# Performance work log

Hardware: AMD Instinct MI355X
Metric: run time of the kernel (lower is better)

The kernel has to match this reference:

```python
import jax, jax.numpy as jnp
import numpy as np

N, E, F_IN, F_E = 50000, 800000, 128, 16
R, H, C = 4, 4, 32            # num_relations, heads, out_channels
HC = H * C                     # 128
NEG_SLOPE = 0.2                # PyG RGATConv default negative_slope
EPS = 1e-16                    # PyG softmax epsilon


def rgat_conv(x, src, dst, edge_type, edge_attr, w, q, k, e, le, b, concat):
    """Faithful PyG RGATConv (additive-self-attention, across-relation, dim=1, aggr=add).
    x: [N,F]; w: [R,F,H*C]; q,k,e: [H*C,H]; le: [F_e,H*C]; b: bias."""
    n = x.shape[0]
    xw = jnp.einsum('nf,rfo->rno', x, w)              # [R,N,H*C] per-relation projections
    x_i = xw[edge_type, dst]                          # [E,H*C] target-node proj per edge
    x_j = xw[edge_type, src]                          # [E,H*C] source-node proj per edge
    qi = x_i @ q                                      # [E,H]
    kj = x_j @ k + (edge_attr @ le) @ e               # [E,H] (edge features folded into keys)
    alpha = jax.nn.leaky_relu(qi + kj, NEG_SLOPE)     # [E,H]
    # softmax over incoming edges of each destination node (across relations)
    amax = jax.ops.segment_max(alpha, dst, num_segments=n)
    ex = jnp.exp(alpha - amax[dst])
    denom = jax.ops.segment_sum(ex, dst, num_segments=n)
    alpha = ex / (denom[dst] + EPS)
    msg = alpha[:, :, None] * x_j.reshape(-1, H, C)   # [E,H,C]
    out = jax.ops.segment_sum(msg, dst, num_segments=n)  # [N,H,C] sum aggregation
    out = out.reshape(n, H * C) if concat else out.mean(axis=1)
    return out + b


def setup_inputs() -> dict:
    key = jax.random.key(0)
    ks = jax.random.split(key, 18)
    p = 0.05
    inp = {
        'x': jax.random.normal(ks[0], (N, F_IN), dtype=jnp.float32),
        'edge_index': jax.random.randint(ks[1], (2, E), 0, N, dtype=jnp.int64)
            if jax.config.jax_enable_x64 else jax.random.randint(ks[1], (2, E), 0, N).astype(jnp.int32),
        'edge_attr': jax.random.normal(ks[2], (E, F_E), dtype=jnp.float32),
        'edge_type': jax.random.randint(ks[3], (E,), 0, R).astype(jnp.int32),
        # conv1 params (in=F_IN, concat=True -> bias of size H*C)
        'w1': jax.random.normal(ks[4], (R, F_IN, HC), dtype=jnp.float32) * p,
        'q1': jax.random.normal(ks[5], (HC, H), dtype=jnp.float32) * p,
        'k1': jax.random.normal(ks[6], (HC, H), dtype=jnp.float32) * p,
        'e1': jax.random.normal(ks[7], (HC, H), dtype=jnp.float32) * p,
        'le1': jax.random.normal(ks[8], (F_E, HC), dtype=jnp.float32) * p,
        'b1': jnp.zeros((HC,), dtype=jnp.float32),
        # conv3 params (in=H*C=128, concat=False -> bias of size C)
        'w3': jax.random.normal(ks[9], (R, HC, HC), dtype=jnp.float32) * p,
        'q3': jax.random.normal(ks[10], (HC, H), dtype=jnp.float32) * p,
        'k3': jax.random.normal(ks[11], (HC, H), dtype=jnp.float32) * p,
        'e3': jax.random.normal(ks[12], (HC, H), dtype=jnp.float32) * p,
        'le3': jax.random.normal(ks[13], (F_E, HC), dtype=jnp.float32) * p,
        'b3': jnp.zeros((C,), dtype=jnp.float32),
    }
    return inp


def reference(x, edge_index, edge_attr, edge_type,
              w1, q1, k1, e1, le1, b1,
              w3, q3, k3, e3, le3, b3):
    src, dst = edge_index[0], edge_index[1]
    h = jax.nn.relu(rgat_conv(x, src, dst, edge_type, edge_attr,
                              w1, q1, k1, e1, le1, b1, concat=True))
    out = rgat_conv(h, src, dst, edge_type, edge_attr,
                    w3, q3, k3, e3, le3, b3, concat=False)
    return out
```

## Files before the change

kernel.cpp:

```cpp
#include <hip/hip_runtime.h>


#define NEG_SLOPE 0.2f
#define SOFT_EPS 1e-16f

typedef __attribute__((ext_vector_type(8))) short bf16x8;
typedef __attribute__((ext_vector_type(4))) float f32x4;
typedef __attribute__((ext_vector_type(4))) unsigned short u16x4;
typedef __attribute__((ext_vector_type(4))) _Float16 half4;
typedef __attribute__((ext_vector_type(8))) _Float16 half8;

__device__ __forceinline__ void bf16split(float f, unsigned short& h, unsigned short& l) {
  unsigned u = __float_as_uint(f);
  unsigned r = u + 0x7FFFu + ((u >> 16) & 1u);
  h = (unsigned short)(r >> 16);
  float fh = __uint_as_float(((unsigned)h) << 16);
  float d = f - fh;
  unsigned u2 = __float_as_uint(d);
  unsigned r2 = u2 + 0x7FFFu + ((u2 >> 16) & 1u);
  l = (unsigned short)(r2 >> 16);
}


__device__ __forceinline__ void hist_body(int id, const int* __restrict__ dst,
                                          int* __restrict__ deg, int E) {
  int e = id * 256 + (int)threadIdx.x;
  if (e < E) atomicAdd(&deg[dst[e]], 1);
}

__device__ __forceinline__ void convx_body(int id, const float* __restrict__ in,
                                           unsigned short* __restrict__ hi,
                                           unsigned short* __restrict__ lo, int total8) {
  int i = id * 256 + (int)threadIdx.x;
  if (i >= total8) return;
  const float4* p = (const float4*)in + (size_t)i * 2;
  float4 a = p[0], b = p[1];
  float v[8] = {a.x, a.y, a.z, a.w, b.x, b.y, b.z, b.w};
  bf16x8 hv, lv;
#pragma unroll
  for (int j = 0; j < 8; ++j) {
    unsigned short h, l;
    bf16split(v[j], h, l);
    hv[j] = (short)h; lv[j] = (short)l;
  }
  *(bf16x8*)(hi + (size_t)i * 8) = hv;
  *(bf16x8*)(lo + (size_t)i * 8) = lv;
}

__device__ __forceinline__ void convw_body(int idx, const float* __restrict__ w1,
                                           const float* __restrict__ w3,
                                           unsigned short* __restrict__ whiT1,
                                           unsigned short* __restrict__ wloT1,
                                           unsigned short* __restrict__ whiT3,
                                           unsigned short* __restrict__ wloT3) {
  if (idx >= 131072) return;
  int L = idx >> 16;
  int rem = idx & 65535;
  int r = rem >> 14, rem2 = rem & 16383, f = rem2 >> 7, o = rem2 & 127;
  const float* w = L ? w3 : w1;
  unsigned short* hiT = L ? whiT3 : whiT1;
  unsigned short* loT = L ? wloT3 : wloT1;
  float v = w[(r * 128 + f) * 128 + o];
  unsigned short h, l;
  bf16split(v, h, l);
  hiT[(r * 128 + o) * 128 + f] = h;
  loT[(r * 128 + o) * 128 + f] = l;
}

__device__ __forceinline__ void wqk_body(int idx, const float* __restrict__ w1,
                                         const float* __restrict__ q1, const float* __restrict__ k1,
                                         const float* __restrict__ w3, const float* __restrict__ q3,
                                         const float* __restrict__ k3, float* __restrict__ wqk) {
  if (idx >= 8192) return;
  int L = idx >> 12, rem = idx & 4095;
  int r = rem >> 10, rem2 = rem & 1023, f = rem2 >> 3, j = rem2 & 7;
  const float* w = L ? w3 : w1;
  const float* qk = (j < 4) ? (L ? q3 : q1) : (L ? k3 : k1);
  int h = j & 3;
  const float* wrow = w + (r * 128 + f) * 128;
  float acc = 0.f;
  for (int o = 0; o < 128; ++o) acc += wrow[o] * qk[o * 4 + h];
  wqk[idx] = acc;
}

__device__ __forceinline__ void lee_body(const float* __restrict__ le1, const float* __restrict__ e1,
                                         const float* __restrict__ le3, const float* __restrict__ e3,
                                         float* __restrict__ lee) {
  int t = threadIdx.x;
  if (t >= 128) return;
  const float* le = (t < 64) ? le1 : le3;
  const float* ee = (t < 64) ? e1 : e3;
  int u = t & 63, f = u >> 2, h = u & 3;
  float acc = 0.f;
  for (int o = 0; o < 128; ++o) acc += le[f * 128 + o] * ee[o * 4 + h];
  lee[t] = acc;
}

__global__ __launch_bounds__(256) void pre_kernel(
    const int* __restrict__ dst, int* __restrict__ deg, int E,
    const float* __restrict__ x, unsigned short* __restrict__ xhi,
    unsigned short* __restrict__ xlo, int total8,
    const float* __restrict__ w1, const float* __restrict__ q1, const float* __restrict__ k1,
    const float* __restrict__ w3, const float* __restrict__ q3, const float* __restrict__ k3,
    float* __restrict__ wqk,
    const float* __restrict__ le1, const float* __restrict__ e1,
    const float* __restrict__ le3, const float* __restrict__ e3, float* __restrict__ lee,
    unsigned short* __restrict__ whiT1, unsigned short* __restrict__ wloT1,
    unsigned short* __restrict__ whiT3, unsigned short* __restrict__ wloT3,
    int nAB, int eb, int cxb) {
  int bid = blockIdx.x;
  if (bid < nAB) {
    int id = bid >> 1;
    if (bid & 1) {
      if (id < eb) hist_body(id, dst, deg, E);
    } else {
      if (id < cxb) convx_body(id, x, xhi, xlo, total8);
    }
  } else {
    int b2 = bid - nAB;
    if (b2 < 512) {
      convw_body(b2 * 256 + (int)threadIdx.x, w1, w3, whiT1, wloT1, whiT3, wloT3);
    } else if (b2 < 544) {
      wqk_body((b2 - 512) * 256 + (int)threadIdx.x, w1, q1, k1, w3, q3, k3, wqk);
    } else {
      lee_body(le1, e1, le3, e3, lee);
    }
  }
}


__global__ __launch_bounds__(256) void scanA_kernel(const int* __restrict__ deg,
                                                    int* __restrict__ bsum, int N) {
  int b = blockIdx.x, t = threadIdx.x;
  int base = b * 1024 + t * 4;
  int s = 0;
#pragma unroll
  for (int j = 0; j < 4; ++j) {
    int i = base + j;
    if (i < N) s += deg[i];
  }
#pragma unroll
  for (int o = 1; o < 64; o <<= 1) s += __shfl_xor(s, o);
  __shared__ int wsum[4];
  if ((t & 63) == 0) wsum[t >> 6] = s;
  __syncthreads();
  if (t == 0) bsum[b] = wsum[0] + wsum[1] + wsum[2] + wsum[3];
}

__global__ __launch_bounds__(256) void scanB_kernel(const int* __restrict__ bsum,
                                                    int* __restrict__ boff,
                                                    int* __restrict__ row_start,
                                                    int nb, int N) {
  int t = threadIdx.x;
  int v = (t < nb) ? bsum[t] : 0;
  int inc = v;
#pragma unroll
  for (int o = 1; o < 64; o <<= 1) {
    int u = __shfl_up(inc, o);
    if ((t & 63) >= o) inc += u;
  }
  __shared__ int wt[4];
  if ((t & 63) == 63) wt[t >> 6] = inc;
  __syncthreads();
  int add = 0;
  for (int wv = 0; wv < (t >> 6); ++wv) add += wt[wv];
  inc += add;
  if (t < nb) boff[t] = inc - v;
  if (t == 255) row_start[N] = inc;
}

__global__ __launch_bounds__(256) void scanC_kernel(const int* __restrict__ deg,
                                                    const int* __restrict__ boff,
                                                    int* __restrict__ row_start,
                                                    int* __restrict__ cursor, int N) {
  int b = blockIdx.x, t = threadIdx.x;
  int base = b * 1024 + t * 4;
  int d[4];
  int s = 0;
#pragma unroll
  for (int j = 0; j < 4; ++j) {
    int i = base + j;
    d[j] = (i < N) ? deg[i] : 0;
    s += d[j];
  }
  int inc = s;
#pragma unroll
  for (int o = 1; o < 64; o <<= 1) {
    int u = __shfl_up(inc, o);
    if ((t & 63) >= o) inc += u;
  }
  __shared__ int wt[4];
  if ((t & 63) == 63) wt[t >> 6] = inc;
  __syncthreads();
  int add = boff[b];
  for (int wv = 0; wv < (t >> 6); ++wv) add += wt[wv];
  int off = add + inc - s;
#pragma unroll
  for (int j = 0; j < 4; ++j) {
    int i = base + j;
    if (i < N) {
      row_start[i] = off;
      cursor[i] = off;
      off += d[j];
    }
  }
}


__device__ __forceinline__ void scatter_body(int id, const int* __restrict__ src,
                                             const int* __restrict__ dst,
                                             const int* __restrict__ et,
                                             int* __restrict__ cursor,
                                             int4* __restrict__ es, int E) {
  int e = id * 256 + (int)threadIdx.x;
  if (e >= E) return;
  int d = dst[e];
  int pos = atomicAdd(&cursor[d], 1);
  es[pos] = make_int4(src[e], d, et[e], e);
}

__device__ __forceinline__ void qkx_body(int nbid, char* smem, const float* __restrict__ xin,
                                         const float* __restrict__ wqk, float* __restrict__ qn,
                                         float* __restrict__ kn, int N) {
  float* sx = (float*)smem;
  float* swqk = sx + 64 * 132;
  int nb = nbid * 64;
  int t = threadIdx.x;
#pragma unroll
  for (int j = 0; j < 16; ++j) {
    int i = j * 256 + t;
    swqk[(i >> 10) * 1032 + (i & 1023)] = wqk[i];
  }
#pragma unroll
  for (int j = 0; j < 8; ++j) {
    int i = j * 256 + t;
    int n = nb + (i >> 5); if (n >= N) n = N - 1;
    ((float4*)sx)[(i >> 5) * 33 + (i & 31)] =
        ((const float4*)(xin + (size_t)n * 128))[i & 31];
  }
  __syncthreads();
  int rl = t >> 2, r = t & 3;
  float aq0 = 0, aq1 = 0, aq2 = 0, aq3 = 0;
  float ak0 = 0, ak1 = 0, ak2 = 0, ak3 = 0;
  const float* xr = sx + rl * 132;
  const float* wb = swqk + r * 1032;
  for (int f = 0; f < 128; ++f) {
    float xv = xr[f];
    float4 qw = *(const float4*)(wb + f * 8);
    float4 kw = *(const float4*)(wb + f * 8 + 4);
    aq0 += xv * qw.x; aq1 += xv * qw.y; aq2 += xv * qw.z; aq3 += xv * qw.w;
    ak0 += xv * kw.x; ak1 += xv * kw.y; ak2 += xv * kw.z; ak3 += xv * kw.w;
  }
  int n = nb + rl;
  if (n < N) {
    *(float4*)(qn + ((size_t)r * N + n) * 4) = make_float4(aq0, aq1, aq2, aq3);
    *(float4*)(kn + ((size_t)r * N + n) * 4) = make_float4(ak0, ak1, ak2, ak3);
  }
}

__global__ __launch_bounds__(256) void sc_kernel(
    const int* __restrict__ src, const int* __restrict__ dst, const int* __restrict__ et,
    int* __restrict__ cursor, int4* __restrict__ es, int E,
    const float* __restrict__ xin, const float* __restrict__ wqk,
    float* __restrict__ qn, float* __restrict__ kn, int N, int qxb) {
  extern __shared__ char smem[];
  int bid = blockIdx.x;
  int g = bid / 5, r5 = bid - g * 5;
  if (r5 == 4) {
    if (g < qxb) qkx_body(g, smem, xin, wqk, qn, kn, N);
  } else {
    scatter_body(g * 4 + r5, src, dst, et, cursor, es, E);
  }
}


__device__ __forceinline__ void ek2_body(int id, char* smem, const int4* __restrict__ es,
                                         const float* __restrict__ ea,
                                         const float* __restrict__ lee,
                                         float* __restrict__ eks1, float* __restrict__ eks3,
                                         int E) {
  float* sl = (float*)smem;
  if (threadIdx.x < 128) sl[threadIdx.x] = lee[threadIdx.x];
  __syncthreads();
  int i = id * 256 + (int)threadIdx.x;
  if (i >= E) return;
  int eid = es[i].w;
  const float4* a4 = (const float4*)(ea + (size_t)eid * 16);
  float a1[4] = {0, 0, 0, 0}, a3[4] = {0, 0, 0, 0};
#pragma unroll
  for (int ii = 0; ii < 4; ++ii) {
    float4 v = a4[ii];
    int f = ii * 4;
#pragma unroll
    for (int h = 0; h < 4; ++h) {
      a1[h] += v.x * sl[f * 4 + h] + v.y * sl[(f + 1) * 4 + h] +
               v.z * sl[(f + 2) * 4 + h] + v.w * sl[(f + 3) * 4 + h];
      a3[h] += v.x * sl[64 + f * 4 + h] + v.y * sl[64 + (f + 1) * 4 + h] +
               v.z * sl[64 + (f + 2) * 4 + h] + v.w * sl[64 + (f + 3) * 4 + h];
    }
  }
  *(float4*)(eks1 + (size_t)i * 4) = make_float4(a1[0], a1[1], a1[2], a1[3]);
  *(float4*)(eks3 + (size_t)i * 4) = make_float4(a3[0], a3[1], a3[2], a3[3]);
}

__device__ __forceinline__ void proj_body(int pid, char* smem,
                                          const unsigned short* __restrict__ xhi,
                                          const unsigned short* __restrict__ xlo,
                                          const unsigned short* __restrict__ whiT,
                                          const unsigned short* __restrict__ wloT,
                                          _Float16* __restrict__ xwh, int N) {
  bf16x8* wl_h = (bf16x8*)smem;
  bf16x8* wl_l = wl_h + 2048;
  int r = pid & 3;
  int nb = (pid >> 2) * 128;
  int t = threadIdx.x;
  const unsigned short* wh = whiT + r * (128 * 128);
  const unsigned short* wl = wloT + r * (128 * 128);

#pragma unroll
  for (int j = 0; j < 8; ++j) {
    int i = j * 256 + t;
    int c = i & 15, q = (i >> 4) & 3, kc = (i >> 6) & 3, ot = i >> 8;
    int srco = (ot * 16 + c) * 128 + kc * 32 + q * 8;
    wl_h[i] = *(const bf16x8*)(wh + srco);
    wl_l[i] = *(const bf16x8*)(wl + srco);
  }
  __syncthreads();

  int wv = t >> 6;
  int lane = t & 63;
  int c = lane & 15, q = lane >> 4;
  int nodebase = nb + wv * 32;
  int n0 = nodebase + c;
  int n1 = nodebase + 16 + c;
  int n0c = n0 < N ? n0 : N - 1;
  int n1c = n1 < N ? n1 : N - 1;

  f32x4 acc[8][2];
#pragma unroll
  for (int ot = 0; ot < 8; ++ot)
#pragma unroll
    for (int nt = 0; nt < 2; ++nt) acc[ot][nt] = (f32x4){0.f, 0.f, 0.f, 0.f};

  bf16x8 xb[2][4];
  {
    int k0 = q * 8;
    xb[0][0] = *(const bf16x8*)(xhi + (size_t)n0c * 128 + k0);
    xb[0][1] = *(const bf16x8*)(xlo + (size_t)n0c * 128 + k0);
    xb[0][2] = *(const bf16x8*)(xhi + (size_t)n1c * 128 + k0);
    xb[0][3] = *(const bf16x8*)(xlo + (size_t)n1c * 128 + k0);
  }
#pragma unroll
  for (int kc = 0; kc < 4; ++kc) {
    if (kc < 3) {
      int k0 = (kc + 1) * 32 + q * 8;
      xb[(kc + 1) & 1][0] = *(const bf16x8*)(xhi + (size_t)n0c * 128 + k0);
      xb[(kc + 1) & 1][1] = *(const bf16x8*)(xlo + (size_t)n0c * 128 + k0);
      xb[(kc + 1) & 1][2] = *(const bf16x8*)(xhi + (size_t)n1c * 128 + k0);
      xb[(kc + 1) & 1][3] = *(const bf16x8*)(xlo + (size_t)n1c * 128 + k0);
    }
    bf16x8 b0h = xb[kc & 1][0], b0l = xb[kc & 1][1];
    bf16x8 b1h = xb[kc & 1][2], b1l = xb[kc & 1][3];
#pragma unroll
    for (int ot = 0; ot < 8; ++ot) {
      int fi = ((ot * 4 + kc) * 4 + q) * 16 + c;
      bf16x8 ah = wl_h[fi];
      bf16x8 al = wl_l[fi];
      acc[ot][0] = __builtin_amdgcn_mfma_f32_16x16x32_bf16(ah, b0h, acc[ot][0], 0, 0, 0);
      acc[ot][0] = __builtin_amdgcn_mfma_f32_16x16x32_bf16(ah, b0l, acc[ot][0], 0, 0, 0);
      acc[ot][0] = __builtin_amdgcn_mfma_f32_16x16x32_bf16(al, b0h, acc[ot][0], 0, 0, 0);
      acc[ot][1] = __builtin_amdgcn_mfma_f32_16x16x32_bf16(ah, b1h, acc[ot][1], 0, 0, 0);
      acc[ot][1] = __builtin_amdgcn_mfma_f32_16x16x32_bf16(ah, b1l, acc[ot][1], 0, 0, 0);
      acc[ot][1] = __builtin_amdgcn_mfma_f32_16x16x32_bf16(al, b1h, acc[ot][1], 0, 0, 0);
    }
  }

#pragma unroll
  for (int nt = 0; nt < 2; ++nt) {
    int n = nodebase + nt * 16 + c;
    if (n < N) {
      _Float16* basep = xwh + ((size_t)r * N + n) * 128 + q * 4;
#pragma unroll
      for (int ot = 0; ot < 8; ++ot) {
        f32x4 a = acc[ot][nt];
        half4 hv;
        hv[0] = (_Float16)a.x; hv[1] = (_Float16)a.y;
        hv[2] = (_Float16)a.z; hv[3] = (_Float16)a.w;
        *(half4*)(basep + ot * 16) = hv;
      }
    }
  }
}

__global__ __launch_bounds__(256) void ep1_kernel(
    const int4* __restrict__ es, const float* __restrict__ ea, const float* __restrict__ lee,
    float* __restrict__ eks1, float* __restrict__ eks3, int E,
    const unsigned short* __restrict__ xhi, const unsigned short* __restrict__ xlo,
    const unsigned short* __restrict__ whiT, const unsigned short* __restrict__ wloT,
    _Float16* __restrict__ xwh, int N, int pjb) {
  extern __shared__ char smem[];
  int bid = blockIdx.x;
  int g = bid / 3, r3 = bid - g * 3;
  if (r3 == 2) {
    if (g < pjb) proj_body(g, smem, xhi, xlo, whiT, wloT, xwh, N);
  } else {
    ek2_body(g * 2 + r3, smem, es, ea, lee, eks1, eks3, E);
  }
}

__global__ __launch_bounds__(256) void p2_kernel(
    const unsigned short* __restrict__ xhi, const unsigned short* __restrict__ xlo,
    const unsigned short* __restrict__ whiT, const unsigned short* __restrict__ wloT,
    _Float16* __restrict__ xwh, int N,
    const float* __restrict__ xin, const float* __restrict__ wqk,
    float* __restrict__ qn, float* __restrict__ kn, int pjb, int qxb) {
  extern __shared__ char smem[];
  int bid = blockIdx.x;
  int g = bid / 3, r3 = bid - g * 3;
  if (r3 == 2) {
    if (g < qxb) qkx_body(g, smem, xin, wqk, qn, kn, N);
  } else {
    int id = g * 2 + r3;
    if (id < pjb) proj_body(id, smem, xhi, xlo, whiT, wloT, xwh, N);
  }
}


__device__ __forceinline__ float4 edge_alpha(const int4* __restrict__ es,
                                             const float* __restrict__ qn,
                                             const float* __restrict__ kn,
                                             const float* __restrict__ eks,
                                             int i, int d, int N) {
  int4 v = es[i];
  float4 kv = *(const float4*)(kn + (v.z * N + v.x) * 4);
  float4 ev = ((const float4*)eks)[i];
  float4 q4 = *(const float4*)(qn + (v.z * N + d) * 4);
  float4 a = make_float4(q4.x + kv.x + ev.x, q4.y + kv.y + ev.y,
                         q4.z + kv.z + ev.z, q4.w + kv.w + ev.w);
  a.x = a.x > 0.f ? a.x : NEG_SLOPE * a.x;
  a.y = a.y > 0.f ? a.y : NEG_SLOPE * a.y;
  a.z = a.z > 0.f ? a.z : NEG_SLOPE * a.z;
  a.w = a.w > 0.f ? a.w : NEG_SLOPE * a.w;
  return a;
}

__device__ __forceinline__ float4 max4(float4 a, float4 b) {
  return make_float4(fmaxf(a.x, b.x), fmaxf(a.y, b.y), fmaxf(a.z, b.z), fmaxf(a.w, b.w));
}

__global__ __launch_bounds__(256) void agg_kernel(
    const int4* __restrict__ es, const int* __restrict__ row_start,
    const float* __restrict__ qn, const float* __restrict__ kn,
    const float* __restrict__ eks, float* __restrict__ alpha_s,
    const _Float16* __restrict__ xwh, const float* __restrict__ bias,
    float* __restrict__ out, unsigned short* __restrict__ xhi,
    unsigned short* __restrict__ xlo, int N, int concat) {
  int d = blockIdx.x * 16 + (threadIdx.x >> 4);
  if (d >= N) return;
  int ql = threadIdx.x & 15;
  int rs = row_start[d], re = row_start[d + 1];
  int deg = re - rs;
  int h = ql >> 2;

  float acc[8];
#pragma unroll
  for (int j = 0; j < 8; ++j) acc[j] = 0.f;
  float rden = 0.f;

  if (deg > 0) {
    float4 m = make_float4(-1e30f, -1e30f, -1e30f, -1e30f);
    float4 ar0 = m, ar1 = m, ar2 = m, ar3 = m;
    bool fast = (deg <= 64);
    bool v0 = ql < deg, v1 = 16 + ql < deg, v2 = 32 + ql < deg, v3 = 48 + ql < deg;
    if (fast) {
      int dm1 = deg - 1;
      int o0 = v0 ? ql : dm1;
      int o1 = v1 ? 16 + ql : dm1;
      int o2 = v2 ? 32 + ql : dm1;
      int o3 = v3 ? 48 + ql : dm1;
      float4 a0 = edge_alpha(es, qn, kn, eks, rs + o0, d, N);
      float4 a1 = edge_alpha(es, qn, kn, eks, rs + o1, d, N);
      float4 a2 = edge_alpha(es, qn, kn, eks, rs + o2, d, N);
      float4 a3 = edge_alpha(es, qn, kn, eks, rs + o3, d, N);
      if (v0) { ar0 = a0; m = max4(m, a0); }
      if (v1) { ar1 = a1; m = max4(m, a1); }
      if (v2) { ar2 = a2; m = max4(m, a2); }
      if (v3) { ar3 = a3; m = max4(m, a3); }
    } else {
      for (int i = rs + ql; i < re; i += 16) {
        float4 a = edge_alpha(es, qn, kn, eks, i, d, N);
        ((float4*)alpha_s)[i] = a;
        m = max4(m, a);
      }
    }
#pragma unroll
    for (int o = 1; o < 16; o <<= 1) {
      m.x = fmaxf(m.x, __shfl_xor(m.x, o));
      m.y = fmaxf(m.y, __shfl_xor(m.y, o));
      m.z = fmaxf(m.z, __shfl_xor(m.z, o));
      m.w = fmaxf(m.w, __shfl_xor(m.w, o));
    }

    float4 s = make_float4(0.f, 0.f, 0.f, 0.f);
    if (fast) {
#define SWEEPB(V, AR, OFF)                                                   \
      if (V) {                                                               \
        float4 e4 = make_float4(__expf(AR.x - m.x), __expf(AR.y - m.y),      \
                                __expf(AR.z - m.z), __expf(AR.w - m.w));     \
        ((float4*)alpha_s)[rs + OFF + ql] = e4;                              \
        s.x += e4.x; s.y += e4.y; s.z += e4.z; s.w += e4.w;                  \
      }
      SWEEPB(v0, ar0, 0)
      SWEEPB(v1, ar1, 16)
      SWEEPB(v2, ar2, 32)
      SWEEPB(v3, ar3, 48)
#undef SWEEPB
    } else {
      for (int i = rs + ql; i < re; i += 16) {
        float4 a = ((const float4*)alpha_s)[i];
        float4 e4 = make_float4(__expf(a.x - m.x), __expf(a.y - m.y),
                                __expf(a.z - m.z), __expf(a.w - m.w));
        ((float4*)alpha_s)[i] = e4;
        s.x += e4.x; s.y += e4.y; s.z += e4.z; s.w += e4.w;
      }
    }
#pragma unroll
    for (int o = 1; o < 16; o <<= 1) {
      s.x += __shfl_xor(s.x, o); s.y += __shfl_xor(s.y, o);
      s.z += __shfl_xor(s.z, o); s.w += __shfl_xor(s.w, o);
    }
    float smh = (h == 0) ? s.x : (h == 1) ? s.y : (h == 2) ? s.z : s.w;
    rden = 1.f / (smh + SOFT_EPS);

    int e = rs;
    for (; e + 4 <= re; e += 4) {
      int4 a0 = es[e];
      int4 a1 = es[e + 1];
      int4 a2 = es[e + 2];
      int4 a3 = es[e + 3];
      float w0 = alpha_s[e * 4 + h];
      float w1 = alpha_s[(e + 1) * 4 + h];
      float w2 = alpha_s[(e + 2) * 4 + h];
      float w3 = alpha_s[(e + 3) * 4 + h];
      half8 x0 = *(const half8*)(xwh + (a0.z * N + a0.x) * 128 + ql * 8);
      half8 x1 = *(const half8*)(xwh + (a1.z * N + a1.x) * 128 + ql * 8);
      half8 x2 = *(const half8*)(xwh + (a2.z * N + a2.x) * 128 + ql * 8);
      half8 x3 = *(const half8*)(xwh + (a3.z * N + a3.x) * 128 + ql * 8);
#pragma unroll
      for (int j = 0; j < 8; ++j) {
        acc[j] = fmaf((float)x0[j], w0, acc[j]);
        acc[j] = fmaf((float)x1[j], w1, acc[j]);
        acc[j] = fmaf((float)x2[j], w2, acc[j]);
        acc[j] = fmaf((float)x3[j], w3, acc[j]);
      }
    }
    for (; e < re; ++e) {
      int4 a0 = es[e];
      float w0 = alpha_s[e * 4 + h];
      half8 x0 = *(const half8*)(xwh + (a0.z * N + a0.x) * 128 + ql * 8);
#pragma unroll
      for (int j = 0; j < 8; ++j) acc[j] = fmaf((float)x0[j], w0, acc[j]);
    }
  }
#pragma unroll
  for (int j = 0; j < 8; ++j) acc[j] *= rden;

  if (concat) {
    float4 b0 = ((const float4*)bias)[ql * 2];
    float4 b1 = ((const float4*)bias)[ql * 2 + 1];
    float v[8] = {acc[0] + b0.x, acc[1] + b0.y, acc[2] + b0.z, acc[3] + b0.w,
                  acc[4] + b1.x, acc[5] + b1.y, acc[6] + b1.z, acc[7] + b1.w};
    u16x4 hv0, lv0, hv1, lv1;
#pragma unroll
    for (int j = 0; j < 8; ++j) {
      v[j] = v[j] > 0.f ? v[j] : 0.f;
      unsigned short hh, ll;
      bf16split(v[j], hh, ll);
      if (j < 4) { hv0[j] = hh; lv0[j] = ll; }
      else { hv1[j - 4] = hh; lv1[j - 4] = ll; }
    }
    float* orow = out + (size_t)d * 128 + ql * 8;
    *(float4*)orow = make_float4(v[0], v[1], v[2], v[3]);
    *(float4*)(orow + 4) = make_float4(v[4], v[5], v[6], v[7]);
    *(u16x4*)(xhi + (size_t)d * 128 + ql * 8) = hv0;
    *(u16x4*)(xhi + (size_t)d * 128 + ql * 8 + 4) = hv1;
    *(u16x4*)(xlo + (size_t)d * 128 + ql * 8) = lv0;
    *(u16x4*)(xlo + (size_t)d * 128 + ql * 8 + 4) = lv1;
  } else {
#pragma unroll
    for (int j = 0; j < 8; ++j) {
      acc[j] += __shfl_xor(acc[j], 4);
      acc[j] += __shfl_xor(acc[j], 8);
    }
    if (ql < 4) {
      float4 b0 = ((const float4*)bias)[ql * 2];
      float4 b1 = ((const float4*)bias)[ql * 2 + 1];
      float* orow = out + (size_t)d * 32 + ql * 8;
      *(float4*)orow = make_float4(0.25f * acc[0] + b0.x, 0.25f * acc[1] + b0.y,
                                   0.25f * acc[2] + b0.z, 0.25f * acc[3] + b0.w);
      *(float4*)(orow + 4) = make_float4(0.25f * acc[4] + b1.x, 0.25f * acc[5] + b1.y,
                                         0.25f * acc[6] + b1.z, 0.25f * acc[7] + b1.w);
    }
  }
}

extern "C" void kernel_launch(void* const* d_in, const int* in_sizes, int n_in,
                              void* d_out, int out_size, void* d_ws, size_t ws_size,
                              hipStream_t stream) {
  const float* x   = (const float*)d_in[0];
  const int*   ei  = (const int*)d_in[1];
  const float* ea  = (const float*)d_in[2];
  const int*   etp = (const int*)d_in[3];
  const float* w1  = (const float*)d_in[4];
  const float* q1  = (const float*)d_in[5];
  const float* k1  = (const float*)d_in[6];
  const float* e1  = (const float*)d_in[7];
  const float* le1 = (const float*)d_in[8];
  const float* b1  = (const float*)d_in[9];
  const float* w3  = (const float*)d_in[10];
  const float* q3  = (const float*)d_in[11];
  const float* k3  = (const float*)d_in[12];
  const float* e3  = (const float*)d_in[13];
  const float* le3 = (const float*)d_in[14];
  const float* b3  = (const float*)d_in[15];
  const int N = in_sizes[0] / 128;
  const int E = in_sizes[3];
  const int* srcp = ei;
  const int* dstp = ei + E;

  float* ws   = (float*)d_ws;
  _Float16* xwh = (_Float16*)ws;
  float* qn   = ws + (size_t)2 * N * 128;
  float* kn   = qn + (size_t)4 * N * 4;
  float* eks1 = kn + (size_t)4 * N * 4;
  float* eks3 = eks1 + (size_t)E * 4;
  float* alph = eks3 + (size_t)E * 4;
  float* hbuf = alph + (size_t)E * 4;
  float* leeb = hbuf + (size_t)N * 128;
  float* wqkb = leeb + 128;
  int* deg      = (int*)(wqkb + 8192);
  int* rowst    = deg + N;
  int* cursor   = rowst + N + 1;
  int* bsum     = cursor + N;
  int* boff     = bsum + 256;
  uintptr_t pe = (uintptr_t)(boff + 256);
  pe = (pe + 15) & ~(uintptr_t)15;
  int4* es      = (int4*)pe;
  uintptr_t pa = (uintptr_t)(es + E);
  pa = (pa + 255) & ~(uintptr_t)255;
  unsigned short* xhi   = (unsigned short*)pa;
  unsigned short* xlo   = xhi + (size_t)N * 128;
  unsigned short* whiT1 = xlo + (size_t)N * 128;
  unsigned short* wloT1 = whiT1 + 4 * 128 * 128;
  unsigned short* whiT3 = wloT1 + 4 * 128 * 128;
  unsigned short* wloT3 = whiT3 + 4 * 128 * 128;
  (void)ws_size; (void)n_in; (void)out_size;

  int eb   = (E + 255) / 256;
  int nb16 = (N + 15) / 16;
  int nbs  = (N + 1023) / 1024;
  int pgy  = (N + 127) / 128;
  int pjb  = 4 * pgy;
  int qxb  = (N + 63) / 64;
  int cxb  = (N * 128 / 8 + 255) / 256;

  hipMemsetAsync(deg, 0, (size_t)N * sizeof(int), stream);

  int M = eb > cxb ? eb : cxb;
  int nAB = 2 * M;
  int preg = nAB + 512 + 32 + 1;
  pre_kernel<<<preg, 256, 0, stream>>>(dstp, deg, E, x, xhi, xlo, N * 128 / 8,
                                       w1, q1, k1, w3, q3, k3, wqkb,
                                       le1, e1, le3, e3, leeb,
                                       whiT1, wloT1, whiT3, wloT3, nAB, eb, cxb);
  scanA_kernel<<<nbs, 256, 0, stream>>>(deg, bsum, N);
  scanB_kernel<<<1, 256, 0, stream>>>(bsum, boff, rowst, nbs, N);
  scanC_kernel<<<nbs, 256, 0, stream>>>(deg, boff, rowst, cursor, N);

  int scq = (eb + 3) / 4;
  int scg = 5 * (scq > qxb ? scq : qxb);
  sc_kernel<<<scg, 256, 50304, stream>>>(srcp, dstp, etp, cursor, es, E,
                                         x, wqkb, qn, kn, N, qxb);

  int ekh = (eb + 1) / 2;
  int e1g = 3 * (ekh > pjb ? ekh : pjb);
  ep1_kernel<<<e1g, 256, 65536, stream>>>(es, ea, leeb, eks1, eks3, E,
                                          xhi, xlo, whiT1, wloT1, xwh, N, pjb);

  agg_kernel<<<nb16, 256, 0, stream>>>(es, rowst, qn, kn, eks1, alph, xwh,
                                       b1, hbuf, xhi, xlo, N, 1);

  int pjh = (pjb + 1) / 2;
  int p2g = 3 * (pjh > qxb ? pjh : qxb);
  p2_kernel<<<p2g, 256, 65536, stream>>>(xhi, xlo, whiT3, wloT3, xwh, N,
                                         hbuf, wqkb + 4096, qn, kn, pjb, qxb);

  agg_kernel<<<nb16, 256, 0, stream>>>(es, rowst, qn, kn, eks3, alph, xwh,
                                       b3, (float*)d_out, xhi, xlo, N, 0);
}
```

Before: 441.0 us.

## Pre-swizzle weights to MFMA fragment order and drop LDS staging to cut shared memory

The bf16 hi/lo weight split is now written directly in the per-lane MFMA fragment layout, so the projection reads A-fragments straight from global/L2 instead of staging 64KB into LDS and syncing. The q/k node projection also reads x rows directly from global memory as float4 instead of staging them in LDS. Dynamic shared memory for the fused kernels drops sharply (65536 to 512 and 16512 bytes), aiming to raise occupancy and overlap the co-scheduled edge and projection blocks. The cost is repeated global reads of the weights per block, relying on cache hits, and uncoalesced per-thread x row reads.

```diff
diff --git a/kernel.cpp b/kernel.cpp
--- a/kernel.cpp
+++ b/kernel.cpp
@@ -49,22 +49,24 @@
 
 __device__ __forceinline__ void convw_body(int idx, const float* __restrict__ w1,
                                            const float* __restrict__ w3,
-                                           unsigned short* __restrict__ whiT1,
-                                           unsigned short* __restrict__ wloT1,
-                                           unsigned short* __restrict__ whiT3,
-                                           unsigned short* __restrict__ wloT3) {
+                                           unsigned short* __restrict__ wF1h,
+                                           unsigned short* __restrict__ wF1l,
+                                           unsigned short* __restrict__ wF3h,
+                                           unsigned short* __restrict__ wF3l) {
   if (idx >= 131072) return;
   int L = idx >> 16;
   int rem = idx & 65535;
   int r = rem >> 14, rem2 = rem & 16383, f = rem2 >> 7, o = rem2 & 127;
   const float* w = L ? w3 : w1;
-  unsigned short* hiT = L ? whiT3 : whiT1;
-  unsigned short* loT = L ? wloT3 : wloT1;
+  unsigned short* dh = L ? wF3h : wF1h;
+  unsigned short* dl = L ? wF3l : wF1l;
   float v = w[(r * 128 + f) * 128 + o];
   unsigned short h, l;
   bf16split(v, h, l);
-  hiT[(r * 128 + o) * 128 + f] = h;
-  loT[(r * 128 + o) * 128 + f] = l;
+  int ot = o >> 4, c = o & 15, kc = f >> 5, q = (f >> 3) & 3, j = f & 7;
+  int di = r * 16384 + ((((ot * 4 + kc) * 4 + q) * 16 + c) * 8 + j);
+  dh[di] = h;
+  dl[di] = l;
 }
 
 __device__ __forceinline__ void wqk_body(int idx, const float* __restrict__ w1,
@@ -105,8 +107,8 @@
     float* __restrict__ wqk,
     const float* __restrict__ le1, const float* __restrict__ e1,
     const float* __restrict__ le3, const float* __restrict__ e3, float* __restrict__ lee,
-    unsigned short* __restrict__ whiT1, unsigned short* __restrict__ wloT1,
-    unsigned short* __restrict__ whiT3, unsigned short* __restrict__ wloT3,
+    unsigned short* __restrict__ wF1h, unsigned short* __restrict__ wF1l,
+    unsigned short* __restrict__ wF3h, unsigned short* __restrict__ wF3l,
     int nAB, int eb, int cxb) {
   int bid = blockIdx.x;
   if (bid < nAB) {
@@ -119,7 +121,7 @@
   } else {
     int b2 = bid - nAB;
     if (b2 < 512) {
-      convw_body(b2 * 256 + (int)threadIdx.x, w1, w3, whiT1, wloT1, whiT3, wloT3);
+      convw_body(b2 * 256 + (int)threadIdx.x, w1, w3, wF1h, wF1l, wF3h, wF3l);
     } else if (b2 < 544) {
       wqk_body((b2 - 512) * 256 + (int)threadIdx.x, w1, q1, k1, w3, q3, k3, wqk);
     } else {
@@ -222,36 +224,43 @@
 __device__ __forceinline__ void qkx_body(int nbid, char* smem, const float* __restrict__ xin,
                                          const float* __restrict__ wqk, float* __restrict__ qn,
                                          float* __restrict__ kn, int N) {
-  float* sx = (float*)smem;
-  float* swqk = sx + 64 * 132;
-  int nb = nbid * 64;
+  float* swqk = (float*)smem;
   int t = threadIdx.x;
 #pragma unroll
   for (int j = 0; j < 16; ++j) {
     int i = j * 256 + t;
     swqk[(i >> 10) * 1032 + (i & 1023)] = wqk[i];
   }
-#pragma unroll
-  for (int j = 0; j < 8; ++j) {
-    int i = j * 256 + t;
-    int n = nb + (i >> 5); if (n >= N) n = N - 1;
-    ((float4*)sx)[(i >> 5) * 33 + (i & 31)] =
-        ((const float4*)(xin + (size_t)n * 128))[i & 31];
-  }
   __syncthreads();
+  int nb = nbid * 64;
   int rl = t >> 2, r = t & 3;
+  int n = nb + rl;
+  int nc = n < N ? n : N - 1;
+  const float4* xr = (const float4*)(xin + (size_t)nc * 128);
+  const float* wb = swqk + r * 1032;
   float aq0 = 0, aq1 = 0, aq2 = 0, aq3 = 0;
   float ak0 = 0, ak1 = 0, ak2 = 0, ak3 = 0;
-  const float* xr = sx + rl * 132;
-  const float* wb = swqk + r * 1032;
-  for (int f = 0; f < 128; ++f) {
-    float xv = xr[f];
-    float4 qw = *(const float4*)(wb + f * 8);
-    float4 kw = *(const float4*)(wb + f * 8 + 4);
-    aq0 += xv * qw.x; aq1 += xv * qw.y; aq2 += xv * qw.z; aq3 += xv * qw.w;
-    ak0 += xv * kw.x; ak1 += xv * kw.y; ak2 += xv * kw.z; ak3 += xv * kw.w;
-  }
-  int n = nb + rl;
+#pragma unroll 4
+  for (int f4 = 0; f4 < 32; ++f4) {
+    float4 xv = xr[f4];
+    const float* w0 = wb + f4 * 32;
+    float4 qa = *(const float4*)(w0);
+    float4 ka = *(const float4*)(w0 + 4);
+    float4 qb = *(const float4*)(w0 + 8);
+    float4 kb = *(const float4*)(w0 + 12);
+    float4 qc = *(const float4*)(w0 + 16);
+    float4 kc = *(const float4*)(w0 + 20);
+    float4 qd = *(const float4*)(w0 + 24);
+    float4 kd = *(const float4*)(w0 + 28);
+    aq0 += xv.x * qa.x + xv.y * qb.x + xv.z * qc.x + xv.w * qd.x;
+    aq1 += xv.x * qa.y + xv.y * qb.y + xv.z * qc.y + xv.w * qd.y;
+    aq2 += xv.x * qa.z + xv.y * qb.z + xv.z * qc.z + xv.w * qd.z;
+    aq3 += xv.x * qa.w + xv.y * qb.w + xv.z * qc.w + xv.w * qd.w;
+    ak0 += xv.x * ka.x + xv.y * kb.x + xv.z * kc.x + xv.w * kd.x;
+    ak1 += xv.x * ka.y + xv.y * kb.y + xv.z * kc.y + xv.w * kd.y;
+    ak2 += xv.x * ka.z + xv.y * kb.z + xv.z * kc.z + xv.w * kd.z;
+    ak3 += xv.x * ka.w + xv.y * kb.w + xv.z * kc.w + xv.w * kd.w;
+  }
   if (n < N) {
     *(float4*)(qn + ((size_t)r * N + n) * 4) = make_float4(aq0, aq1, aq2, aq3);
     *(float4*)(kn + ((size_t)r * N + n) * 4) = make_float4(ak0, ak1, ak2, ak3);
@@ -303,33 +312,20 @@
   *(float4*)(eks3 + (size_t)i * 4) = make_float4(a3[0], a3[1], a3[2], a3[3]);
 }
 
-__device__ __forceinline__ void proj_body(int pid, char* smem,
+__device__ __forceinline__ void proj_body(int pid,
                                           const unsigned short* __restrict__ xhi,
                                           const unsigned short* __restrict__ xlo,
-                                          const unsigned short* __restrict__ whiT,
-                                          const unsigned short* __restrict__ wloT,
+                                          const unsigned short* __restrict__ wFh,
+                                          const unsigned short* __restrict__ wFl,
                                           _Float16* __restrict__ xwh, int N) {
-  bf16x8* wl_h = (bf16x8*)smem;
-  bf16x8* wl_l = wl_h + 2048;
   int r = pid & 3;
   int nb = (pid >> 2) * 128;
   int t = threadIdx.x;
-  const unsigned short* wh = whiT + r * (128 * 128);
-  const unsigned short* wl = wloT + r * (128 * 128);
-
-#pragma unroll
-  for (int j = 0; j < 8; ++j) {
-    int i = j * 256 + t;
-    int c = i & 15, q = (i >> 4) & 3, kc = (i >> 6) & 3, ot = i >> 8;
-    int srco = (ot * 16 + c) * 128 + kc * 32 + q * 8;
-    wl_h[i] = *(const bf16x8*)(wh + srco);
-    wl_l[i] = *(const bf16x8*)(wl + srco);
-  }
-  __syncthreads();
-
   int wv = t >> 6;
   int lane = t & 63;
   int c = lane & 15, q = lane >> 4;
+  const bf16x8* whp = (const bf16x8*)(wFh + r * 16384) + lane;
+  const bf16x8* wlp = (const bf16x8*)(wFl + r * 16384) + lane;
   int nodebase = nb + wv * 32;
   int n0 = nodebase + c;
   int n1 = nodebase + 16 + c;
@@ -363,9 +359,8 @@
     bf16x8 b1h = xb[kc & 1][2], b1l = xb[kc & 1][3];
 #pragma unroll
     for (int ot = 0; ot < 8; ++ot) {
-      int fi = ((ot * 4 + kc) * 4 + q) * 16 + c;
-      bf16x8 ah = wl_h[fi];
-      bf16x8 al = wl_l[fi];
+      bf16x8 ah = whp[(ot * 4 + kc) * 64];
+      bf16x8 al = wlp[(ot * 4 + kc) * 64];
       acc[ot][0] = __builtin_amdgcn_mfma_f32_16x16x32_bf16(ah, b0h, acc[ot][0], 0, 0, 0);
       acc[ot][0] = __builtin_amdgcn_mfma_f32_16x16x32_bf16(ah, b0l, acc[ot][0], 0, 0, 0);
       acc[ot][0] = __builtin_amdgcn_mfma_f32_16x16x32_bf16(al, b0h, acc[ot][0], 0, 0, 0);
@@ -396,13 +391,13 @@
     const int4* __restrict__ es, const float* __restrict__ ea, const float* __restrict__ lee,
     float* __restrict__ eks1, float* __restrict__ eks3, int E,
     const unsigned short* __restrict__ xhi, const unsigned short* __restrict__ xlo,
-    const unsigned short* __restrict__ whiT, const unsigned short* __restrict__ wloT,
+    const unsigned short* __restrict__ wFh, const unsigned short* __restrict__ wFl,
     _Float16* __restrict__ xwh, int N, int pjb) {
   extern __shared__ char smem[];
   int bid = blockIdx.x;
   int g = bid / 3, r3 = bid - g * 3;
   if (r3 == 2) {
-    if (g < pjb) proj_body(g, smem, xhi, xlo, whiT, wloT, xwh, N);
+    if (g < pjb) proj_body(g, xhi, xlo, wFh, wFl, xwh, N);
   } else {
     ek2_body(g * 2 + r3, smem, es, ea, lee, eks1, eks3, E);
   }
@@ -410,7 +405,7 @@
 
 __global__ __launch_bounds__(256) void p2_kernel(
     const unsigned short* __restrict__ xhi, const unsigned short* __restrict__ xlo,
-    const unsigned short* __restrict__ whiT, const unsigned short* __restrict__ wloT,
+    const unsigned short* __restrict__ wFh, const unsigned short* __restrict__ wFl,
     _Float16* __restrict__ xwh, int N,
     const float* __restrict__ xin, const float* __restrict__ wqk,
     float* __restrict__ qn, float* __restrict__ kn, int pjb, int qxb) {
@@ -421,7 +416,7 @@
     if (g < qxb) qkx_body(g, smem, xin, wqk, qn, kn, N);
   } else {
     int id = g * 2 + r3;
-    if (id < pjb) proj_body(id, smem, xhi, xlo, whiT, wloT, xwh, N);
+    if (id < pjb) proj_body(id, xhi, xlo, wFh, wFl, xwh, N);
   }
 }
 
@@ -648,12 +643,12 @@
   int4* es      = (int4*)pe;
   uintptr_t pa = (uintptr_t)(es + E);
   pa = (pa + 255) & ~(uintptr_t)255;
-  unsigned short* xhi   = (unsigned short*)pa;
-  unsigned short* xlo   = xhi + (size_t)N * 128;
-  unsigned short* whiT1 = xlo + (size_t)N * 128;
-  unsigned short* wloT1 = whiT1 + 4 * 128 * 128;
-  unsigned short* whiT3 = wloT1 + 4 * 128 * 128;
-  unsigned short* wloT3 = whiT3 + 4 * 128 * 128;
+  unsigned short* xhi  = (unsigned short*)pa;
+  unsigned short* xlo  = xhi + (size_t)N * 128;
+  unsigned short* wF1h = xlo + (size_t)N * 128;
+  unsigned short* wF1l = wF1h + 4 * 128 * 128;
+  unsigned short* wF3h = wF1l + 4 * 128 * 128;
+  unsigned short* wF3l = wF3h + 4 * 128 * 128;
   (void)ws_size; (void)n_in; (void)out_size;
 
   int eb   = (E + 255) / 256;
@@ -672,27 +667,27 @@
   pre_kernel<<<preg, 256, 0, stream>>>(dstp, deg, E, x, xhi, xlo, N * 128 / 8,
                                        w1, q1, k1, w3, q3, k3, wqkb,
                                        le1, e1, le3, e3, leeb,
-                                       whiT1, wloT1, whiT3, wloT3, nAB, eb, cxb);
+                                       wF1h, wF1l, wF3h, wF3l, nAB, eb, cxb);
   scanA_kernel<<<nbs, 256, 0, stream>>>(deg, bsum, N);
   scanB_kernel<<<1, 256, 0, stream>>>(bsum, boff, rowst, nbs, N);
   scanC_kernel<<<nbs, 256, 0, stream>>>(deg, boff, rowst, cursor, N);
 
   int scq = (eb + 3) / 4;
   int scg = 5 * (scq > qxb ? scq : qxb);
-  sc_kernel<<<scg, 256, 50304, stream>>>(srcp, dstp, etp, cursor, es, E,
+  sc_kernel<<<scg, 256, 16512, stream>>>(srcp, dstp, etp, cursor, es, E,
                                          x, wqkb, qn, kn, N, qxb);
 
   int ekh = (eb + 1) / 2;
   int e1g = 3 * (ekh > pjb ? ekh : pjb);
-  ep1_kernel<<<e1g, 256, 65536, stream>>>(es, ea, leeb, eks1, eks3, E,
-                                          xhi, xlo, whiT1, wloT1, xwh, N, pjb);
+  ep1_kernel<<<e1g, 256, 512, stream>>>(es, ea, leeb, eks1, eks3, E,
+                                        xhi, xlo, wF1h, wF1l, xwh, N, pjb);
 
   agg_kernel<<<nb16, 256, 0, stream>>>(es, rowst, qn, kn, eks1, alph, xwh,
                                        b1, hbuf, xhi, xlo, N, 1);
 
   int pjh = (pjb + 1) / 2;
   int p2g = 3 * (pjh > qxb ? pjh : qxb);
-  p2_kernel<<<p2g, 256, 65536, stream>>>(xhi, xlo, whiT3, wloT3, xwh, N,
+  p2_kernel<<<p2g, 256, 16512, stream>>>(xhi, xlo, wF3h, wF3l, xwh, N,
                                          hbuf, wqkb + 4096, qn, kn, pjb, qxb);
 
   agg_kernel<<<nb16, 256, 0, stream>>>(es, rowst, qn, kn, eks3, alph, xwh,
```

After: 479.3 us. +8.7%, slower.
